# Optimization experiments

Measured on AMD Instinct MI355X. Metric: run time of the kernel, lower is better.

Reference implementation:

```python
import jax, jax.numpy as jnp
import numpy as np

N_NODES = 100000
N_EDGES = 1600000
IN_CH = 16
HID = 128
N_LAYERS = 4
OUT_CH = 3


def setup_inputs() -> dict:
    key = jax.random.key(0)
    ks = jax.random.split(key, 8)
    x = jax.random.normal(ks[0], (N_NODES, IN_CH), dtype=jnp.float32)
    edge_index = jax.random.randint(ks[1], (2, N_EDGES), 0, N_NODES, dtype=jnp.int64)
    # glorot-ish scaled params
    enc_W = jax.random.normal(ks[2], (IN_CH, HID), dtype=jnp.float32) * (1.0 / np.sqrt(IN_CH))
    enc_b = jnp.zeros((HID,), dtype=jnp.float32)
    conv_W = jax.random.normal(ks[3], (N_LAYERS, HID, HID), dtype=jnp.float32) * (1.0 / np.sqrt(HID))
    conv_b = jnp.zeros((N_LAYERS, HID), dtype=jnp.float32)
    dec_W = jax.random.normal(ks[4], (HID, OUT_CH), dtype=jnp.float32) * (1.0 / np.sqrt(HID))
    dec_b = jnp.zeros((OUT_CH,), dtype=jnp.float32)
    return {"x": x, "edge_index": edge_index, "enc_W": enc_W, "enc_b": enc_b,
            "conv_W": conv_W, "conv_b": conv_b, "dec_W": dec_W, "dec_b": dec_b}


def _gcn_forward(x, edge_index, enc_W, enc_b, conv_W, conv_b, dec_W, dec_b):
    n = x.shape[0]
    # PyG GCNConv: add self-loops, symmetric deg^-1/2 normalization
    loops = jnp.arange(n, dtype=edge_index.dtype)
    src = jnp.concatenate([edge_index[0], loops])  # [E+N]
    dst = jnp.concatenate([edge_index[1], loops])  # [E+N]
    deg = jax.ops.segment_sum(jnp.ones_like(dst, dtype=x.dtype), dst, num_segments=n)
    dinv = jnp.where(deg > 0, jax.lax.rsqrt(deg), 0.0)
    norm = (dinv[src] * dinv[dst])[:, None]  # [E+N, 1]

    h = jax.nn.relu(x @ enc_W + enc_b)  # encoder + ReLU
    for l in range(conv_W.shape[0]):
        hw = h @ conv_W[l]                      # [N, H] transform
        msg = hw[src] * norm                    # gather + normalize
        h = jax.ops.segment_sum(msg, dst, num_segments=n) + conv_b[l]
        h = jax.nn.relu(h)
    return h @ dec_W + dec_b  # decoder [N, 3]


def reference(x, edge_index, enc_W, enc_b, conv_W, conv_b, dec_W, dec_b):
    return _gcn_forward(x, edge_index, enc_W, enc_b, conv_W, conv_b, dec_W, dec_b)
```

## Files before the change

kernel.cpp:

```cpp
#include <hip/hip_runtime.h>


typedef float f32x4 __attribute__((ext_vector_type(4)));
typedef _Float16 h8 __attribute__((ext_vector_type(8)));

#define BKT_CAP 6144


__global__ __launch_bounds__(256) void k_bin(const int* __restrict__ src, const int* __restrict__ dst,
                                             int* __restrict__ bcnt, unsigned* __restrict__ ebuf, int E, int NB) {
  __shared__ int hist[512];
  __shared__ int lofs[512];
  int tid = threadIdx.x;
  int base = blockIdx.x * 4096;
  for (int i = tid; i < NB; i += 256) hist[i] = 0;
  __syncthreads();
  unsigned rec[16];
  int bk[16];
#pragma unroll
  for (int j = 0; j < 16; j++) {
    int e = base + j * 256 + tid;
    bk[j] = -1;
    if (e < E) {
      int d = dst[e];
      rec[j] = ((unsigned)(d & 255) << 24) | (unsigned)src[e];
      bk[j] = d >> 8;
      atomicAdd(&hist[bk[j]], 1);
    }
  }
  __syncthreads();
  for (int i = tid; i < NB; i += 256) {
    int c = hist[i];
    lofs[i] = c ? atomicAdd(&bcnt[i], c) : 0;
    hist[i] = 0;
  }
  __syncthreads();
#pragma unroll
  for (int j = 0; j < 16; j++) {
    if (bk[j] >= 0) {
      int p = lofs[bk[j]] + atomicAdd(&hist[bk[j]], 1);
      if (p < BKT_CAP) ebuf[(size_t)bk[j] * BKT_CAP + p] = rec[j];
    }
  }
}

__global__ __launch_bounds__(256) void k_bucket_hist(const unsigned* __restrict__ ebuf, const int* __restrict__ bcnt,
                                                     int* __restrict__ cnt, int N) {
  __shared__ int h[256];
  int b = blockIdx.x, tid = threadIdx.x;
  h[tid] = 0;
  __syncthreads();
  int n = min(bcnt[b], BKT_CAP);
  const unsigned* eb = ebuf + (size_t)b * BKT_CAP;
  for (int i = tid; i < n; i += 256) atomicAdd(&h[eb[i] >> 24], 1);
  __syncthreads();
  int d = (b << 8) + tid;
  if (d < N) cnt[d] = h[tid];
}

__global__ __launch_bounds__(256) void k_bucket_fill(const unsigned* __restrict__ ebuf, const int* __restrict__ bcnt,
                                                     const int* __restrict__ rp, int* __restrict__ col, int N) {
  __shared__ int h[256];
  int b = blockIdx.x, tid = threadIdx.x;
  h[tid] = 0;
  __syncthreads();
  int n = min(bcnt[b], BKT_CAP);
  const unsigned* eb = ebuf + (size_t)b * BKT_CAP;
  for (int i = tid; i < n; i += 256) {
    unsigned r = eb[i];
    int dlow = r >> 24;
    int pos = rp[(b << 8) + dlow] + atomicAdd(&h[dlow], 1);
    col[pos] = (int)(r & 0xFFFFFFu);
  }
}


__global__ __launch_bounds__(256) void k_scan_local(const int* __restrict__ cnt, int* __restrict__ rp,
                                                    int* __restrict__ bsums, int N) {
  int base = blockIdx.x * 4096 + threadIdx.x * 16;
  int v[16];
#pragma unroll
  for (int j = 0; j < 16; j++) { int i = base + j; v[j] = (i < N) ? cnt[i] : 0; }
  int tsum = 0;
#pragma unroll
  for (int j = 0; j < 16; j++) tsum += v[j];
  int l = threadIdx.x & 63, w = threadIdx.x >> 6;
  int s = tsum;
#pragma unroll
  for (int off = 1; off < 64; off <<= 1) { int t = __shfl_up(s, off); if (l >= off) s += t; }
  __shared__ int wsum[4];
  if (l == 63) wsum[w] = s;
  __syncthreads();
  int woff = 0;
  for (int i = 0; i < w; i++) woff += wsum[i];
  int run = woff + s - tsum;
#pragma unroll
  for (int j = 0; j < 16; j++) { int i = base + j; if (i < N) rp[i] = run; run += v[j]; }
  if (threadIdx.x == 255) bsums[blockIdx.x] = woff + s;
}

__global__ void k_scan_sums(const int* __restrict__ bsums, int* __restrict__ bsex,
                            int* __restrict__ rp, int nsb, int N) {
  if (threadIdx.x == 0 && blockIdx.x == 0) {
    int run = 0;
    for (int i = 0; i < nsb; i++) { bsex[i] = run; run += bsums[i]; }
    rp[N] = run;
  }
}

__global__ __launch_bounds__(256) void k_scan_add(const int* __restrict__ cnt, int* __restrict__ rp,
                                                  const int* __restrict__ bsex, float* __restrict__ dinv, int N) {
  int i = blockIdx.x * blockDim.x + threadIdx.x;
  if (i >= N) return;
  rp[i] = rp[i] + bsex[i >> 12];
  dinv[i] = 1.0f / sqrtf((float)(cnt[i] + 1));
}

__global__ __launch_bounds__(128) void k_prep_w(const float* __restrict__ convW, _Float16* __restrict__ Whi,
                                                _Float16* __restrict__ Wlo) {
  int lk = blockIdx.x;
  int l = lk >> 7, k = lk & 127, c = threadIdx.x;
  float x = convW[((size_t)l * 128 + k) * 128 + c];
  _Float16 hi = (_Float16)x;
  _Float16 lo = (_Float16)((x - (float)hi) * 2048.0f);
  size_t o = ((size_t)l * 128 + c) * 128 + k;
  Whi[o] = hi;
  Wlo[o] = lo;
}


__global__ __launch_bounds__(256) void k_encoder(const float* __restrict__ x, const float* __restrict__ W,
                                                 const float* __restrict__ b, _Float16* __restrict__ H, int N) {
  int node = blockIdx.x * 2 + (threadIdx.x >> 7);
  int c = threadIdx.x & 127;
  if (node >= N) return;
  const float* xr = x + (size_t)node * 16;
  float acc = b[c];
#pragma unroll
  for (int k = 0; k < 16; k++) acc = fmaf(xr[k], W[k * 128 + c], acc);
  H[(size_t)node * 128 + c] = (_Float16)fmaxf(acc, 0.0f);
}

__global__ __launch_bounds__(512) void k_gemm_mfma(const _Float16* __restrict__ A, const _Float16* __restrict__ Whi,
                                                   const _Float16* __restrict__ Wlo, const float* __restrict__ dinv,
                                                   _Float16* __restrict__ B, int N) {
  __shared__ __align__(16) ushort lds[3 * 128 * 64];
  const int tid = threadIdx.x;
  const int row0 = blockIdx.x * 128;
  const int w = tid >> 6, l = tid & 63;
  const int wm = w >> 1, wn = w & 1;
  const int lr = l & 15, lg = l >> 4;

  f32x4 zero4 = {0.0f, 0.0f, 0.0f, 0.0f};
  f32x4 acc[2][4], acc2[2][4];
#pragma unroll
  for (int m = 0; m < 2; m++)
#pragma unroll
    for (int n = 0; n < 4; n++) { acc[m][n] = zero4; acc2[m][n] = zero4; }

  for (int half = 0; half < 2; half++) {
    uint4 v[6];
#pragma unroll
    for (int i = 0; i < 6; i++) {
      int g = tid + i * 512;
      int region = g >> 10;
      int idx = g & 1023;
      int row = idx >> 3;
      int c16 = idx & 7;
      const _Float16* srcb;
      int grow = row;
      bool valid = true;
      if (region == 0) { srcb = A; grow = row0 + row; valid = grow < N; }
      else if (region == 1) { srcb = Whi; }
      else { srcb = Wlo; }
      v[i] = valid ? *reinterpret_cast<const uint4*>(srcb + (size_t)grow * 128 + half * 64 + c16 * 8)
                   : uint4{0u, 0u, 0u, 0u};
    }
    if (half) __syncthreads();
#pragma unroll
    for (int i = 0; i < 6; i++) {
      int g = tid + i * 512;
      int region = g >> 10;
      int idx = g & 1023;
      int row = idx >> 3;
      int c16 = idx & 7;
      int byte_off = region * 16384 + ((row * 128 + c16 * 16) ^ ((row & 7) << 4));
      *reinterpret_cast<uint4*>(reinterpret_cast<char*>(lds) + byte_off) = v[i];
    }
    __syncthreads();

#pragma unroll
    for (int ksl = 0; ksl < 2; ksl++) {
      int kb = (ksl * 32 + lg * 8) * 2;
      h8 ah[2];
#pragma unroll
      for (int m = 0; m < 2; m++) {
        int row = wm * 32 + m * 16 + lr;
        int off = (row * 128 + kb) ^ ((row & 7) << 4);
        ah[m] = *reinterpret_cast<const h8*>(reinterpret_cast<char*>(lds) + off);
      }
      h8 wh[4], wl[4];
#pragma unroll
      for (int n = 0; n < 4; n++) {
        int colr = wn * 64 + n * 16 + lr;
        int off = (colr * 128 + kb) ^ ((colr & 7) << 4);
        wh[n] = *reinterpret_cast<const h8*>(reinterpret_cast<char*>(lds) + 16384 + off);
        wl[n] = *reinterpret_cast<const h8*>(reinterpret_cast<char*>(lds) + 32768 + off);
      }
#pragma unroll
      for (int m = 0; m < 2; m++)
#pragma unroll
        for (int n = 0; n < 4; n++) {
          acc2[m][n] = __builtin_amdgcn_mfma_f32_16x16x32_f16(ah[m], wl[n], acc2[m][n], 0, 0, 0);
          acc[m][n]  = __builtin_amdgcn_mfma_f32_16x16x32_f16(ah[m], wh[n], acc[m][n], 0, 0, 0);
        }
    }
  }

#pragma unroll
  for (int m = 0; m < 2; m++) {
    int rbase = row0 + wm * 32 + m * 16 + lg * 4;
#pragma unroll
    for (int r = 0; r < 4; r++) {
      int grow = rbase + r;
      if (grow < N) {
        float s = dinv[grow];
#pragma unroll
        for (int n = 0; n < 4; n++) {
          int colc = wn * 64 + n * 16 + lr;
          float val = acc[m][n][r] + 4.8828125e-4f * acc2[m][n][r];
          B[(size_t)grow * 128 + colc] = (_Float16)(val * s);
        }
      }
    }
  }
}

__global__ __launch_bounds__(256) void k_aggregate(const _Float16* __restrict__ B, const int* __restrict__ rp,
                                                   const int* __restrict__ col, const float* __restrict__ dinv,
                                                   const float* __restrict__ bias, _Float16* __restrict__ H, int N) {
  int w = threadIdx.x >> 6, l = threadIdx.x & 63;
  int d = blockIdx.x * 4 + w;
  if (d >= N) return;
  int g = l >> 4, c16 = l & 15;
  int choff = c16 * 8;

  h8 pacc = {(_Float16)0, (_Float16)0, (_Float16)0, (_Float16)0,
             (_Float16)0, (_Float16)0, (_Float16)0, (_Float16)0};

  if (g == 0)
    pacc += *reinterpret_cast<const h8*>(B + (size_t)d * 128 + choff);

  int e0 = rp[d], e1 = rp[d + 1];
  int e = e0 + g;
  for (; e + 12 < e1; e += 16) {
    int s0 = col[e], s1 = col[e + 4], s2 = col[e + 8], s3 = col[e + 12];
    h8 v0 = *reinterpret_cast<const h8*>(B + (size_t)s0 * 128 + choff);
    h8 v1 = *reinterpret_cast<const h8*>(B + (size_t)s1 * 128 + choff);
    h8 v2 = *reinterpret_cast<const h8*>(B + (size_t)s2 * 128 + choff);
    h8 v3 = *reinterpret_cast<const h8*>(B + (size_t)s3 * 128 + choff);
    h8 t01 = v0 + v1;
    h8 t23 = v2 + v3;
    pacc += t01 + t23;
  }
  for (; e < e1; e += 4) {
    int s0 = col[e];
    pacc += *reinterpret_cast<const h8*>(B + (size_t)s0 * 128 + choff);
  }

  float acc[8];
#pragma unroll
  for (int j = 0; j < 8; j++) acc[j] = (float)pacc[j];
#pragma unroll
  for (int j = 0; j < 8; j++) acc[j] += __shfl_xor(acc[j], 32);
#pragma unroll
  for (int j = 0; j < 8; j++) acc[j] += __shfl_xor(acc[j], 16);

  if (g == 0) {
    float dv = dinv[d];
    h8 ov;
#pragma unroll
    for (int j = 0; j < 8; j++)
      ov[j] = (_Float16)fmaxf(fmaf(dv, acc[j], bias[choff + j]), 0.0f);
    *reinterpret_cast<h8*>(&H[(size_t)d * 128 + choff]) = ov;
  }
}

__global__ __launch_bounds__(256) void k_decoder(const _Float16* __restrict__ H, const float* __restrict__ W,
                                                 const float* __restrict__ b, float* __restrict__ out, int N) {
  int w = threadIdx.x >> 6, l = threadIdx.x & 63;
  int node = blockIdx.x * 4 + w;
  if (node >= N) return;
  size_t base = (size_t)node * 128;
  float h0 = (float)H[base + l];
  float h1 = (float)H[base + 64 + l];
  float s0 = h0 * W[l * 3 + 0] + h1 * W[(l + 64) * 3 + 0];
  float s1 = h0 * W[l * 3 + 1] + h1 * W[(l + 64) * 3 + 1];
  float s2 = h0 * W[l * 3 + 2] + h1 * W[(l + 64) * 3 + 2];
#pragma unroll
  for (int o = 32; o > 0; o >>= 1) {
    s0 += __shfl_down(s0, o);
    s1 += __shfl_down(s1, o);
    s2 += __shfl_down(s2, o);
  }
  if (l == 0) {
    out[(size_t)node * 3 + 0] = s0 + b[0];
    out[(size_t)node * 3 + 1] = s1 + b[1];
    out[(size_t)node * 3 + 2] = s2 + b[2];
  }
}

extern "C" void kernel_launch(void* const* d_in, const int* in_sizes, int n_in,
                              void* d_out, int out_size, void* d_ws, size_t ws_size,
                              hipStream_t stream) {
  const float* x     = (const float*)d_in[0];
  const int*   ei    = (const int*)d_in[1];
  const float* encW  = (const float*)d_in[2];
  const float* encb  = (const float*)d_in[3];
  const float* convW = (const float*)d_in[4];
  const float* convb = (const float*)d_in[5];
  const float* decW  = (const float*)d_in[6];
  const float* decb  = (const float*)d_in[7];
  const int N = in_sizes[0] / 16;
  const int E = in_sizes[1] / 2;
  const int L = in_sizes[4] / (128 * 128);
  const int* src = ei;
  const int* dst = ei + E;
  const int NB = (N + 255) >> 8;

  char* p = (char*)d_ws;
  auto alloc = [&](size_t bytes) -> void* {
    void* q = (void*)p;
    p += (bytes + 255) & ~(size_t)255;
    return q;
  };
  int nsb = (N + 4095) >> 12;
  int*       cnt    = (int*)alloc((size_t)N * 4);
  int*       rp     = (int*)alloc((size_t)(N + 1) * 4);
  int*       bsums  = (int*)alloc((size_t)nsb * 4);
  int*       bsex   = (int*)alloc((size_t)nsb * 4);
  int*       bcnt   = (int*)alloc((size_t)NB * 4);
  float*     dinv   = (float*)alloc((size_t)N * 4);
  int*       colA   = (int*)alloc((size_t)E * 4);
  _Float16*  Hh     = (_Float16*)alloc((size_t)N * 128 * 2);
  size_t bh_bytes   = (size_t)N * 128 * 2;
  size_t ebuf_bytes = (size_t)NB * BKT_CAP * 4;
  void*  bh_union   = alloc(bh_bytes > ebuf_bytes ? bh_bytes : ebuf_bytes);
  _Float16* Bh      = (_Float16*)bh_union;
  unsigned* ebuf    = (unsigned*)bh_union;
  _Float16*  Whi    = (_Float16*)alloc((size_t)L * 128 * 128 * 2);
  _Float16*  Wlo    = (_Float16*)alloc((size_t)L * 128 * 128 * 2);

  hipMemsetAsync(bcnt, 0, (size_t)NB * 4, stream);
  k_bin<<<(E + 4095) / 4096, 256, 0, stream>>>(src, dst, bcnt, ebuf, E, NB);
  k_bucket_hist<<<NB, 256, 0, stream>>>(ebuf, bcnt, cnt, N);
  k_scan_local<<<nsb, 256, 0, stream>>>(cnt, rp, bsums, N);
  k_scan_sums<<<1, 1, 0, stream>>>(bsums, bsex, rp, nsb, N);
  k_scan_add<<<(N + 255) / 256, 256, 0, stream>>>(cnt, rp, bsex, dinv, N);
  k_bucket_fill<<<NB, 256, 0, stream>>>(ebuf, bcnt, rp, colA, N);
  k_prep_w<<<L * 128, 128, 0, stream>>>(convW, Whi, Wlo);
  k_encoder<<<(N + 1) / 2, 256, 0, stream>>>(x, encW, encb, Hh, N);
  int gblocks = (N + 127) / 128;
  for (int l = 0; l < L; l++) {
    k_gemm_mfma<<<gblocks, 512, 0, stream>>>(Hh, Whi + (size_t)l * 128 * 128,
                                             Wlo + (size_t)l * 128 * 128, dinv, Bh, N);
    k_aggregate<<<(N + 3) / 4, 256, 0, stream>>>(Bh, rp, colA, dinv, convb + l * 128, Hh, N);
  }
  k_decoder<<<(N + 3) / 4, 256, 0, stream>>>(Hh, decW, decb, (float*)d_out, N);
}
```

Baseline: 542.9 us.

## Slice transformed features into 16-channel planes and merge CSR build kernels

The GEMM output is written as eight channel-slice planes of 16 halves per node, and aggregation runs one block per (128-node group, slice), with two threads per node each gathering 16 bytes per neighbor. Each slice plane is 1/8 the size of the full feature matrix, so the gathers are meant to hit better in cache. Separately, the CSR construction folds the bucket histogram, prefix scan, dinv computation and fill into one per-bucket kernel plus a tiny serial bucket scan, removing several launches and the intermediate count array. The risks are narrower per-thread work with serial per-edge loops, the GEMM's scattered 2-byte stores into the sliced layout, and a CSR build that assumes no bucket overflows its capacity.

Result: slower. 674.8 us (+24.3%).

```diff
diff --git a/kernel.cpp b/kernel.cpp
--- a/kernel.cpp
+++ b/kernel.cpp
@@ -44,76 +44,52 @@
   }
 }
 
-__global__ __launch_bounds__(256) void k_bucket_hist(const unsigned* __restrict__ ebuf, const int* __restrict__ bcnt,
-                                                     int* __restrict__ cnt, int N) {
+__global__ void k_bscan(const int* __restrict__ bcnt, int* __restrict__ bbase,
+                        int* __restrict__ rp, int NB, int N, int E) {
+  if (threadIdx.x == 0 && blockIdx.x == 0) {
+    int run = 0;
+    for (int i = 0; i < NB; i++) { bbase[i] = run; run += bcnt[i]; }
+    rp[N] = E;
+  }
+}
+
+__global__ __launch_bounds__(256) void k_bfill(const unsigned* __restrict__ ebuf, const int* __restrict__ bcnt,
+                                               const int* __restrict__ bbase, int* __restrict__ rp,
+                                               float* __restrict__ dinv, int* __restrict__ col, int N) {
   __shared__ int h[256];
+  __shared__ int wsum[4];
   int b = blockIdx.x, tid = threadIdx.x;
   h[tid] = 0;
   __syncthreads();
   int n = min(bcnt[b], BKT_CAP);
+  int bb = bbase[b];
   const unsigned* eb = ebuf + (size_t)b * BKT_CAP;
   for (int i = tid; i < n; i += 256) atomicAdd(&h[eb[i] >> 24], 1);
   __syncthreads();
+  int cntv = h[tid];
+  int l = tid & 63, wv = tid >> 6;
+  int s = cntv;
+#pragma unroll
+  for (int off = 1; off < 64; off <<= 1) { int t = __shfl_up(s, off); if (l >= off) s += t; }
+  if (l == 63) wsum[wv] = s;
+  __syncthreads();
+  int woff = 0;
+  for (int i = 0; i < wv; i++) woff += wsum[i];
+  int lpre = woff + s - cntv;
   int d = (b << 8) + tid;
-  if (d < N) cnt[d] = h[tid];
-}
-
-__global__ __launch_bounds__(256) void k_bucket_fill(const unsigned* __restrict__ ebuf, const int* __restrict__ bcnt,
-                                                     const int* __restrict__ rp, int* __restrict__ col, int N) {
-  __shared__ int h[256];
-  int b = blockIdx.x, tid = threadIdx.x;
-  h[tid] = 0;
-  __syncthreads();
-  int n = min(bcnt[b], BKT_CAP);
-  const unsigned* eb = ebuf + (size_t)b * BKT_CAP;
+  if (d < N) {
+    rp[d] = bb + lpre;
+    dinv[d] = 1.0f / sqrtf((float)(cntv + 1));
+  }
+  __syncthreads();
+  h[tid] = lpre;
+  __syncthreads();
   for (int i = tid; i < n; i += 256) {
     unsigned r = eb[i];
     int dlow = r >> 24;
-    int pos = rp[(b << 8) + dlow] + atomicAdd(&h[dlow], 1);
+    int pos = bb + atomicAdd(&h[dlow], 1);
     col[pos] = (int)(r & 0xFFFFFFu);
   }
-}
-
-
-__global__ __launch_bounds__(256) void k_scan_local(const int* __restrict__ cnt, int* __restrict__ rp,
-                                                    int* __restrict__ bsums, int N) {
-  int base = blockIdx.x * 4096 + threadIdx.x * 16;
-  int v[16];
-#pragma unroll
-  for (int j = 0; j < 16; j++) { int i = base + j; v[j] = (i < N) ? cnt[i] : 0; }
-  int tsum = 0;
-#pragma unroll
-  for (int j = 0; j < 16; j++) tsum += v[j];
-  int l = threadIdx.x & 63, w = threadIdx.x >> 6;
-  int s = tsum;
-#pragma unroll
-  for (int off = 1; off < 64; off <<= 1) { int t = __shfl_up(s, off); if (l >= off) s += t; }
-  __shared__ int wsum[4];
-  if (l == 63) wsum[w] = s;
-  __syncthreads();
-  int woff = 0;
-  for (int i = 0; i < w; i++) woff += wsum[i];
-  int run = woff + s - tsum;
-#pragma unroll
-  for (int j = 0; j < 16; j++) { int i = base + j; if (i < N) rp[i] = run; run += v[j]; }
-  if (threadIdx.x == 255) bsums[blockIdx.x] = woff + s;
-}
-
-__global__ void k_scan_sums(const int* __restrict__ bsums, int* __restrict__ bsex,
-                            int* __restrict__ rp, int nsb, int N) {
-  if (threadIdx.x == 0 && blockIdx.x == 0) {
-    int run = 0;
-    for (int i = 0; i < nsb; i++) { bsex[i] = run; run += bsums[i]; }
-    rp[N] = run;
-  }
-}
-
-__global__ __launch_bounds__(256) void k_scan_add(const int* __restrict__ cnt, int* __restrict__ rp,
-                                                  const int* __restrict__ bsex, float* __restrict__ dinv, int N) {
-  int i = blockIdx.x * blockDim.x + threadIdx.x;
-  if (i >= N) return;
-  rp[i] = rp[i] + bsex[i >> 12];
-  dinv[i] = 1.0f / sqrtf((float)(cnt[i] + 1));
 }
 
 __global__ __launch_bounds__(128) void k_prep_w(const float* __restrict__ convW, _Float16* __restrict__ Whi,
@@ -143,7 +119,7 @@
 
 __global__ __launch_bounds__(512) void k_gemm_mfma(const _Float16* __restrict__ A, const _Float16* __restrict__ Whi,
                                                    const _Float16* __restrict__ Wlo, const float* __restrict__ dinv,
-                                                   _Float16* __restrict__ B, int N) {
+                                                   _Float16* __restrict__ Bs, int N) {
   __shared__ __align__(16) ushort lds[3 * 128 * 64];
   const int tid = threadIdx.x;
   const int row0 = blockIdx.x * 128;
@@ -227,63 +203,52 @@
         float s = dinv[grow];
 #pragma unroll
         for (int n = 0; n < 4; n++) {
-          int colc = wn * 64 + n * 16 + lr;
+          int slice = wn * 4 + n;
           float val = acc[m][n][r] + 4.8828125e-4f * acc2[m][n][r];
-          B[(size_t)grow * 128 + colc] = (_Float16)(val * s);
+          Bs[((size_t)slice * N + grow) * 16 + lr] = (_Float16)(val * s);
         }
       }
     }
   }
 }
 
-__global__ __launch_bounds__(256) void k_aggregate(const _Float16* __restrict__ B, const int* __restrict__ rp,
+__global__ __launch_bounds__(256) void k_aggregate(const _Float16* __restrict__ Bs, const int* __restrict__ rp,
                                                    const int* __restrict__ col, const float* __restrict__ dinv,
                                                    const float* __restrict__ bias, _Float16* __restrict__ H, int N) {
-  int w = threadIdx.x >> 6, l = threadIdx.x & 63;
-  int d = blockIdx.x * 4 + w;
+  int bid = blockIdx.x;
+  int slice = bid & 7;
+  int d = (bid >> 3) * 128 + (threadIdx.x >> 1);
   if (d >= N) return;
-  int g = l >> 4, c16 = l & 15;
-  int choff = c16 * 8;
-
-  h8 pacc = {(_Float16)0, (_Float16)0, (_Float16)0, (_Float16)0,
-             (_Float16)0, (_Float16)0, (_Float16)0, (_Float16)0};
-
-  if (g == 0)
-    pacc += *reinterpret_cast<const h8*>(B + (size_t)d * 128 + choff);
+  int hh = threadIdx.x & 1;
+  const _Float16* base = Bs + (size_t)slice * N * 16 + hh * 8;
+
+  h8 a0 = {(_Float16)0, (_Float16)0, (_Float16)0, (_Float16)0,
+           (_Float16)0, (_Float16)0, (_Float16)0, (_Float16)0};
+  h8 a1 = a0, a2 = a0, a3 = a0;
+
+  a0 += *reinterpret_cast<const h8*>(base + (size_t)d * 16);
 
   int e0 = rp[d], e1 = rp[d + 1];
-  int e = e0 + g;
-  for (; e + 12 < e1; e += 16) {
-    int s0 = col[e], s1 = col[e + 4], s2 = col[e + 8], s3 = col[e + 12];
-    h8 v0 = *reinterpret_cast<const h8*>(B + (size_t)s0 * 128 + choff);
-    h8 v1 = *reinterpret_cast<const h8*>(B + (size_t)s1 * 128 + choff);
-    h8 v2 = *reinterpret_cast<const h8*>(B + (size_t)s2 * 128 + choff);
-    h8 v3 = *reinterpret_cast<const h8*>(B + (size_t)s3 * 128 + choff);
-    h8 t01 = v0 + v1;
-    h8 t23 = v2 + v3;
-    pacc += t01 + t23;
-  }
-  for (; e < e1; e += 4) {
-    int s0 = col[e];
-    pacc += *reinterpret_cast<const h8*>(B + (size_t)s0 * 128 + choff);
-  }
-
-  float acc[8];
-#pragma unroll
-  for (int j = 0; j < 8; j++) acc[j] = (float)pacc[j];
-#pragma unroll
-  for (int j = 0; j < 8; j++) acc[j] += __shfl_xor(acc[j], 32);
-#pragma unroll
-  for (int j = 0; j < 8; j++) acc[j] += __shfl_xor(acc[j], 16);
-
-  if (g == 0) {
-    float dv = dinv[d];
-    h8 ov;
-#pragma unroll
-    for (int j = 0; j < 8; j++)
-      ov[j] = (_Float16)fmaxf(fmaf(dv, acc[j], bias[choff + j]), 0.0f);
-    *reinterpret_cast<h8*>(&H[(size_t)d * 128 + choff]) = ov;
-  }
+  int e = e0;
+  for (; e + 3 < e1; e += 4) {
+    int s0 = col[e], s1 = col[e + 1], s2 = col[e + 2], s3 = col[e + 3];
+    a0 += *reinterpret_cast<const h8*>(base + (size_t)s0 * 16);
+    a1 += *reinterpret_cast<const h8*>(base + (size_t)s1 * 16);
+    a2 += *reinterpret_cast<const h8*>(base + (size_t)s2 * 16);
+    a3 += *reinterpret_cast<const h8*>(base + (size_t)s3 * 16);
+  }
+  for (; e < e1; e++)
+    a1 += *reinterpret_cast<const h8*>(base + (size_t)col[e] * 16);
+
+  float dv = dinv[d];
+  int choff = slice * 16 + hh * 8;
+  h8 ov;
+#pragma unroll
+  for (int j = 0; j < 8; j++) {
+    float sum = ((float)a0[j] + (float)a1[j]) + ((float)a2[j] + (float)a3[j]);
+    ov[j] = (_Float16)fmaxf(fmaf(dv, sum, bias[choff + j]), 0.0f);
+  }
+  *reinterpret_cast<h8*>(&H[(size_t)d * 128 + choff]) = ov;
 }
 
 __global__ __launch_bounds__(256) void k_decoder(const _Float16* __restrict__ H, const float* __restrict__ W,
@@ -334,37 +299,32 @@
     p += (bytes + 255) & ~(size_t)255;
     return q;
   };
-  int nsb = (N + 4095) >> 12;
-  int*       cnt    = (int*)alloc((size_t)N * 4);
   int*       rp     = (int*)alloc((size_t)(N + 1) * 4);
-  int*       bsums  = (int*)alloc((size_t)nsb * 4);
-  int*       bsex   = (int*)alloc((size_t)nsb * 4);
   int*       bcnt   = (int*)alloc((size_t)NB * 4);
+  int*       bbase  = (int*)alloc((size_t)NB * 4);
   float*     dinv   = (float*)alloc((size_t)N * 4);
   int*       colA   = (int*)alloc((size_t)E * 4);
   _Float16*  Hh     = (_Float16*)alloc((size_t)N * 128 * 2);
-  size_t bh_bytes   = (size_t)N * 128 * 2;
+  size_t bs_bytes   = (size_t)N * 128 * 2;
   size_t ebuf_bytes = (size_t)NB * BKT_CAP * 4;
-  void*  bh_union   = alloc(bh_bytes > ebuf_bytes ? bh_bytes : ebuf_bytes);
-  _Float16* Bh      = (_Float16*)bh_union;
-  unsigned* ebuf    = (unsigned*)bh_union;
+  void*  bs_union   = alloc(bs_bytes > ebuf_bytes ? bs_bytes : ebuf_bytes);
+  _Float16* Bs      = (_Float16*)bs_union;
+  unsigned* ebuf    = (unsigned*)bs_union;
   _Float16*  Whi    = (_Float16*)alloc((size_t)L * 128 * 128 * 2);
   _Float16*  Wlo    = (_Float16*)alloc((size_t)L * 128 * 128 * 2);
 
   hipMemsetAsync(bcnt, 0, (size_t)NB * 4, stream);
   k_bin<<<(E + 4095) / 4096, 256, 0, stream>>>(src, dst, bcnt, ebuf, E, NB);
-  k_bucket_hist<<<NB, 256, 0, stream>>>(ebuf, bcnt, cnt, N);
-  k_scan_local<<<nsb, 256, 0, stream>>>(cnt, rp, bsums, N);
-  k_scan_sums<<<1, 1, 0, stream>>>(bsums, bsex, rp, nsb, N);
-  k_scan_add<<<(N + 255) / 256, 256, 0, stream>>>(cnt, rp, bsex, dinv, N);
-  k_bucket_fill<<<NB, 256, 0, stream>>>(ebuf, bcnt, rp, colA, N);
+  k_bscan<<<1, 1, 0, stream>>>(bcnt, bbase, rp, NB, N, E);
+  k_bfill<<<NB, 256, 0, stream>>>(ebuf, bcnt, bbase, rp, dinv, colA, N);
   k_prep_w<<<L * 128, 128, 0, stream>>>(convW, Whi, Wlo);
   k_encoder<<<(N + 1) / 2, 256, 0, stream>>>(x, encW, encb, Hh, N);
   int gblocks = (N + 127) / 128;
+  int ablocks = 8 * ((N + 127) / 128);
   for (int l = 0; l < L; l++) {
     k_gemm_mfma<<<gblocks, 512, 0, stream>>>(Hh, Whi + (size_t)l * 128 * 128,
-                                             Wlo + (size_t)l * 128 * 128, dinv, Bh, N);
-    k_aggregate<<<(N + 3) / 4, 256, 0, stream>>>(Bh, rp, colA, dinv, convb + l * 128, Hh, N);
+                                             Wlo + (size_t)l * 128 * 128, dinv, Bs, N);
+    k_aggregate<<<ablocks, 256, 0, stream>>>(Bs, rp, colA, dinv, convb + l * 128, Hh, N);
   }
   k_decoder<<<(N + 3) / 4, 256, 0, stream>>>(Hh, decW, decb, (float*)d_out, N);
 }
```
